# Kernel optimization log

Measured on AMD Instinct MI355X. Metric: run time of the kernel, lower is better.

## Reference

```python
import jax, jax.numpy as jnp
import numpy as np

N, M, D = 8192, 8192, 64

def softplus(x):
    # transform_forward in pmf-automl
    return jnp.logaddexp(x, 0.0)

def inv_softplus(y):
    # transform_backward: log(exp(y) - 1), stable form
    return y + jnp.log(-jnp.expm1(-y))

def setup_inputs() -> dict:
    key = jax.random.key(0)
    k1, k2 = jax.random.split(key)
    X = jax.random.normal(k1, (N, D), dtype=jnp.float32)
    X2 = jax.random.normal(k2, (M, D), dtype=jnp.float32)
    # raw (pre-softplus) parameters, matching torch init: softplus(raw)=1
    lengthscale = jnp.full((1, D), inv_softplus(jnp.float32(1.0)), dtype=jnp.float32)
    variance = jnp.full((1,), inv_softplus(jnp.float32(1.0)), dtype=jnp.float32)
    return {"X": X, "X2": X2, "lengthscale": lengthscale, "variance": variance}

def reference(X, X2, lengthscale, variance):
    l = softplus(lengthscale)           # [1, D]
    v = softplus(variance)              # [1]
    Xl = X / l                          # [N, D]
    X2l = X2 / l                        # [M, D]
    xn = jnp.sum(Xl * Xl, axis=1)       # [N]
    yn = jnp.sum(X2l * X2l, axis=1)     # [M]
    cross = Xl @ X2l.T                  # [N, M]
    d2 = jnp.maximum(xn[:, None] + yn[None, :] - 2.0 * cross, 0.0)
    return v[0] * jnp.exp(-0.5 * d2)
```

## Files before the change

### kernel.cpp

```cpp
#include <hip/hip_runtime.h>
#include <math.h>

#define NN 8192
#define MM 8192
#define DD 64
#define BM 128
#define BN 128
#define STR 72

typedef __bf16 bf16x8 __attribute__((ext_vector_type(8)));
typedef __bf16 bf16x4 __attribute__((ext_vector_type(4)));
typedef float f32x4 __attribute__((ext_vector_type(4)));

__device__ __forceinline__ float softplus_f(float x) {
    return fmaxf(x, 0.0f) + log1pf(exp2f(-fabsf(x) * 1.4426950408889634f));
}

__global__ __launch_bounds__(256, 2)
void rbf_mfma_kernel(const float* __restrict__ X, const float* __restrict__ X2,
                     const float* __restrict__ raw_l, const float* __restrict__ raw_v,
                     float* __restrict__ out) {
    __shared__ __bf16 Ah[BM][STR];
    __shared__ __bf16 Al[BM][STR];
    __shared__ __bf16 Bh[BN][STR];
    __shared__ __bf16 Bl[BN][STR];
    __shared__ float ls[DD];
    __shared__ float xn[BM];
    __shared__ float yn[BN];

    const int t  = threadIdx.x;
    const int bn = blockIdx.x;
    const int bm = blockIdx.y;

    if (t < DD) ls[t] = 1.0f / softplus_f(raw_l[t]);
    __syncthreads();

    const int k4 = t & 15;
    const int r0 = t >> 4;
    const float il0 = ls[4 * k4 + 0];
    const float il1 = ls[4 * k4 + 1];
    const float il2 = ls[4 * k4 + 2];
    const float il3 = ls[4 * k4 + 3];

    const float* Xb  = X  + (size_t)(bm * BM) * DD;
    const float* X2b = X2 + (size_t)(bn * BN) * DD;

#pragma unroll
    for (int r = 0; r < 8; ++r) {
        const int row = r0 + 16 * r;
        {
            float4 a = *(const float4*)(Xb + row * DD + 4 * k4);
            a.x *= il0; a.y *= il1; a.z *= il2; a.w *= il3;
            bf16x4 h, l;
            h[0] = (__bf16)a.x; l[0] = (__bf16)(a.x - (float)h[0]);
            h[1] = (__bf16)a.y; l[1] = (__bf16)(a.y - (float)h[1]);
            h[2] = (__bf16)a.z; l[2] = (__bf16)(a.z - (float)h[2]);
            h[3] = (__bf16)a.w; l[3] = (__bf16)(a.w - (float)h[3]);
            *(bf16x4*)&Ah[row][4 * k4] = h;
            *(bf16x4*)&Al[row][4 * k4] = l;
        }
        {
            float4 b = *(const float4*)(X2b + row * DD + 4 * k4);
            b.x *= il0; b.y *= il1; b.z *= il2; b.w *= il3;
            bf16x4 h, l;
            h[0] = (__bf16)b.x; l[0] = (__bf16)(b.x - (float)h[0]);
            h[1] = (__bf16)b.y; l[1] = (__bf16)(b.y - (float)h[1]);
            h[2] = (__bf16)b.z; l[2] = (__bf16)(b.z - (float)h[2]);
            h[3] = (__bf16)b.w; l[3] = (__bf16)(b.w - (float)h[3]);
            *(bf16x4*)&Bh[row][4 * k4] = h;
            *(bf16x4*)&Bl[row][4 * k4] = l;
        }
    }

    {
        const int rowl = t & 127;
        const float* p = (t < 128) ? (Xb + rowl * DD) : (X2b + rowl * DD);
        float s = 0.0f;
#pragma unroll
        for (int j = 0; j < 16; ++j) {
            float4 a = *(const float4*)(p + 4 * j);
            float e;
            e = a.x * ls[4 * j + 0]; s = fmaf(e, e, s);
            e = a.y * ls[4 * j + 1]; s = fmaf(e, e, s);
            e = a.z * ls[4 * j + 2]; s = fmaf(e, e, s);
            e = a.w * ls[4 * j + 3]; s = fmaf(e, e, s);
        }
        if (t < 128) xn[rowl] = s; else yn[rowl] = s;
    }
    __syncthreads();

    const int lane = t & 63;
    const int q    = lane >> 4;
    const int r16  = lane & 15;
    const int w    = t >> 6;
    const int row0 = (w >> 1) * 64;
    const int col0 = (w & 1) * 64;

    f32x4 acc[4][4];
#pragma unroll
    for (int mi = 0; mi < 4; ++mi)
#pragma unroll
        for (int ni = 0; ni < 4; ++ni)
#pragma unroll
            for (int r = 0; r < 4; ++r) acc[mi][ni][r] = 0.0f;

#pragma unroll
    for (int kc = 0; kc < 2; ++kc) {
        const int k0 = kc * 32 + q * 8;
        bf16x8 ah[4], al[4], bh[4], bl[4];
#pragma unroll
        for (int i = 0; i < 4; ++i) {
            ah[i] = *(const bf16x8*)&Ah[row0 + i * 16 + r16][k0];
            al[i] = *(const bf16x8*)&Al[row0 + i * 16 + r16][k0];
            bh[i] = *(const bf16x8*)&Bh[col0 + i * 16 + r16][k0];
            bl[i] = *(const bf16x8*)&Bl[col0 + i * 16 + r16][k0];
        }
#pragma unroll
        for (int mi = 0; mi < 4; ++mi) {
#pragma unroll
            for (int ni = 0; ni < 4; ++ni) {
                acc[mi][ni] = __builtin_amdgcn_mfma_f32_16x16x32_bf16(ah[mi], bh[ni], acc[mi][ni], 0, 0, 0);
                acc[mi][ni] = __builtin_amdgcn_mfma_f32_16x16x32_bf16(ah[mi], bl[ni], acc[mi][ni], 0, 0, 0);
                acc[mi][ni] = __builtin_amdgcn_mfma_f32_16x16x32_bf16(al[mi], bh[ni], acc[mi][ni], 0, 0, 0);
            }
        }
    }

    const float v  = softplus_f(raw_v[0]);
    const float ce = -0.5f * 1.4426950408889634f;

#pragma unroll
    for (int mi = 0; mi < 4; ++mi) {
#pragma unroll
        for (int r = 0; r < 4; ++r) {
            const int lrow = row0 + mi * 16 + q * 4 + r;
            const float xr = xn[lrow];
            float* orow = out + (size_t)(bm * BM + lrow) * MM + bn * BN;
#pragma unroll
            for (int ni = 0; ni < 4; ++ni) {
                const int lcol = col0 + ni * 16 + r16;
                float d2 = fmaxf(xr + yn[lcol] - 2.0f * acc[mi][ni][r], 0.0f);
                orow[lcol] = v * exp2f(ce * d2);
            }
        }
    }
}

extern "C" void kernel_launch(void* const* d_in, const int* in_sizes, int n_in,
                              void* d_out, int out_size, void* d_ws, size_t ws_size,
                              hipStream_t stream) {
    const float* X     = (const float*)d_in[0];
    const float* X2    = (const float*)d_in[1];
    const float* raw_l = (const float*)d_in[2];
    const float* raw_v = (const float*)d_in[3];
    float* out = (float*)d_out;

    dim3 grid(MM / BN, NN / BM);
    dim3 block(256);
    rbf_mfma_kernel<<<grid, block, 0, stream>>>(X, X2, raw_l, raw_v, out);
}
```

Measured before the change: 325.6 us.

## Precompute scaled bf16 hi/lo splits and norms in a prep kernel, stage output via LDS

A separate prep kernel scales X and X2 by the inverse lengthscale once, splits each into bf16 hi/lo parts, and computes the row norms into global scratch buffers. The GEMM kernel then reads its MFMA operands straight from global memory, with no per-tile conversion and no LDS operand staging. Operands are swapped in the MFMA so each lane holds contiguous output columns. Results go through a swizzled per-wave LDS tile so stores are coalesced 16-byte writes. This removes redundant per-block conversion work and the scattered 4-byte output stores, at the cost of an extra launch, global scratch traffic, and uncached-by-LDS operand loads.

```diff
diff --git a/kernel.cpp b/kernel.cpp
--- a/kernel.cpp
+++ b/kernel.cpp
@@ -6,95 +6,72 @@
 #define DD 64
 #define BM 128
 #define BN 128
-#define STR 72
 
 typedef __bf16 bf16x8 __attribute__((ext_vector_type(8)));
 typedef __bf16 bf16x4 __attribute__((ext_vector_type(4)));
 typedef float f32x4 __attribute__((ext_vector_type(4)));
 
+__device__ __align__(16) __bf16 g_Xh[(size_t)NN * DD];
+__device__ __align__(16) __bf16 g_Xl[(size_t)NN * DD];
+__device__ __align__(16) __bf16 g_Yh[(size_t)MM * DD];
+__device__ __align__(16) __bf16 g_Yl[(size_t)MM * DD];
+__device__ __align__(16) float  g_xn[NN];
+__device__ __align__(16) float  g_yn[MM];
+
 __device__ __forceinline__ float softplus_f(float x) {
     return fmaxf(x, 0.0f) + log1pf(exp2f(-fabsf(x) * 1.4426950408889634f));
 }
 
-__global__ __launch_bounds__(256, 2)
-void rbf_mfma_kernel(const float* __restrict__ X, const float* __restrict__ X2,
-                     const float* __restrict__ raw_l, const float* __restrict__ raw_v,
-                     float* __restrict__ out) {
-    __shared__ __bf16 Ah[BM][STR];
-    __shared__ __bf16 Al[BM][STR];
-    __shared__ __bf16 Bh[BN][STR];
-    __shared__ __bf16 Bl[BN][STR];
+__global__ __launch_bounds__(64)
+void prep_kernel(const float* __restrict__ X, const float* __restrict__ X2,
+                 const float* __restrict__ raw_l) {
     __shared__ float ls[DD];
-    __shared__ float xn[BM];
-    __shared__ float yn[BN];
-
-    const int t  = threadIdx.x;
-    const int bn = blockIdx.x;
-    const int bm = blockIdx.y;
-
-    if (t < DD) ls[t] = 1.0f / softplus_f(raw_l[t]);
+    const int t = threadIdx.x;
+    ls[t] = 1.0f / softplus_f(raw_l[t]);
     __syncthreads();
 
-    const int k4 = t & 15;
-    const int r0 = t >> 4;
-    const float il0 = ls[4 * k4 + 0];
-    const float il1 = ls[4 * k4 + 1];
-    const float il2 = ls[4 * k4 + 2];
-    const float il3 = ls[4 * k4 + 3];
+    const int row = blockIdx.x * 64 + t;
+    const bool isX = row < NN;
+    const int r = isX ? row : row - NN;
+    const float* src = (isX ? X : X2) + (size_t)r * DD;
+    __bf16* dh = (isX ? g_Xh : g_Yh) + (size_t)r * DD;
+    __bf16* dl = (isX ? g_Xl : g_Yl) + (size_t)r * DD;
 
-    const float* Xb  = X  + (size_t)(bm * BM) * DD;
-    const float* X2b = X2 + (size_t)(bn * BN) * DD;
+    float s = 0.0f;
+#pragma unroll
+    for (int j = 0; j < 16; ++j) {
+        float4 a = *(const float4*)(src + 4 * j);
+        a.x *= ls[4 * j + 0];
+        a.y *= ls[4 * j + 1];
+        a.z *= ls[4 * j + 2];
+        a.w *= ls[4 * j + 3];
+        bf16x4 h, l;
+        h[0] = (__bf16)a.x; l[0] = (__bf16)(a.x - (float)h[0]);
+        h[1] = (__bf16)a.y; l[1] = (__bf16)(a.y - (float)h[1]);
+        h[2] = (__bf16)a.z; l[2] = (__bf16)(a.z - (float)h[2]);
+        h[3] = (__bf16)a.w; l[3] = (__bf16)(a.w - (float)h[3]);
+        *(bf16x4*)(dh + 4 * j) = h;
+        *(bf16x4*)(dl + 4 * j) = l;
+        s = fmaf(a.x, a.x, s);
+        s = fmaf(a.y, a.y, s);
+        s = fmaf(a.z, a.z, s);
+        s = fmaf(a.w, a.w, s);
+    }
+    if (isX) g_xn[r] = s; else g_yn[r] = s;
+}
 
-#pragma unroll
-    for (int r = 0; r < 8; ++r) {
-        const int row = r0 + 16 * r;
-        {
-            float4 a = *(const float4*)(Xb + row * DD + 4 * k4);
-            a.x *= il0; a.y *= il1; a.z *= il2; a.w *= il3;
-            bf16x4 h, l;
-            h[0] = (__bf16)a.x; l[0] = (__bf16)(a.x - (float)h[0]);
-            h[1] = (__bf16)a.y; l[1] = (__bf16)(a.y - (float)h[1]);
-            h[2] = (__bf16)a.z; l[2] = (__bf16)(a.z - (float)h[2]);
-            h[3] = (__bf16)a.w; l[3] = (__bf16)(a.w - (float)h[3]);
-            *(bf16x4*)&Ah[row][4 * k4] = h;
-            *(bf16x4*)&Al[row][4 * k4] = l;
-        }
-        {
-            float4 b = *(const float4*)(X2b + row * DD + 4 * k4);
-            b.x *= il0; b.y *= il1; b.z *= il2; b.w *= il3;
-            bf16x4 h, l;
-            h[0] = (__bf16)b.x; l[0] = (__bf16)(b.x - (float)h[0]);
-            h[1] = (__bf16)b.y; l[1] = (__bf16)(b.y - (float)h[1]);
-            h[2] = (__bf16)b.z; l[2] = (__bf16)(b.z - (float)h[2]);
-            h[3] = (__bf16)b.w; l[3] = (__bf16)(b.w - (float)h[3]);
-            *(bf16x4*)&Bh[row][4 * k4] = h;
-            *(bf16x4*)&Bl[row][4 * k4] = l;
-        }
-    }
+__global__ __launch_bounds__(256, 2)
+void rbf_gemm_kernel(const float* __restrict__ raw_v, float* __restrict__ out) {
+    __shared__ __align__(16) float ctile[4][64 * 64];
 
-    {
-        const int rowl = t & 127;
-        const float* p = (t < 128) ? (Xb + rowl * DD) : (X2b + rowl * DD);
-        float s = 0.0f;
-#pragma unroll
-        for (int j = 0; j < 16; ++j) {
-            float4 a = *(const float4*)(p + 4 * j);
-            float e;
-            e = a.x * ls[4 * j + 0]; s = fmaf(e, e, s);
-            e = a.y * ls[4 * j + 1]; s = fmaf(e, e, s);
-            e = a.z * ls[4 * j + 2]; s = fmaf(e, e, s);
-            e = a.w * ls[4 * j + 3]; s = fmaf(e, e, s);
-        }
-        if (t < 128) xn[rowl] = s; else yn[rowl] = s;
-    }
-    __syncthreads();
-
+    const int t    = threadIdx.x;
     const int lane = t & 63;
+    const int w    = t >> 6;
     const int q    = lane >> 4;
     const int r16  = lane & 15;
-    const int w    = t >> 6;
-    const int row0 = (w >> 1) * 64;
-    const int col0 = (w & 1) * 64;
+
+    const int row0 = blockIdx.y * BM + (w >> 1) * 64;
+    const int col0 = blockIdx.x * BN + (w & 1) * 64;
 
     f32x4 acc[4][4];
 #pragma unroll
@@ -102,47 +79,70 @@
 #pragma unroll
         for (int ni = 0; ni < 4; ++ni)
 #pragma unroll
-            for (int r = 0; r < 4; ++r) acc[mi][ni][r] = 0.0f;
+            for (int rr = 0; rr < 4; ++rr) acc[mi][ni][rr] = 0.0f;
+
+    const char* Xh = (const char*)g_Xh;
+    const char* Xl = (const char*)g_Xl;
+    const char* Yh = (const char*)g_Yh;
+    const char* Yl = (const char*)g_Yl;
 
 #pragma unroll
     for (int kc = 0; kc < 2; ++kc) {
-        const int k0 = kc * 32 + q * 8;
+        const int kb = kc * 64 + q * 16;
         bf16x8 ah[4], al[4], bh[4], bl[4];
 #pragma unroll
         for (int i = 0; i < 4; ++i) {
-            ah[i] = *(const bf16x8*)&Ah[row0 + i * 16 + r16][k0];
-            al[i] = *(const bf16x8*)&Al[row0 + i * 16 + r16][k0];
-            bh[i] = *(const bf16x8*)&Bh[col0 + i * 16 + r16][k0];
-            bl[i] = *(const bf16x8*)&Bl[col0 + i * 16 + r16][k0];
+            const size_t ao = (size_t)(row0 + i * 16 + r16) * 128 + kb;
+            const size_t bo = (size_t)(col0 + i * 16 + r16) * 128 + kb;
+            ah[i] = *(const bf16x8*)(Xh + ao);
+            al[i] = *(const bf16x8*)(Xl + ao);
+            bh[i] = *(const bf16x8*)(Yh + bo);
+            bl[i] = *(const bf16x8*)(Yl + bo);
         }
 #pragma unroll
-        for (int mi = 0; mi < 4; ++mi) {
+        for (int mi = 0; mi < 4; ++mi)
 #pragma unroll
             for (int ni = 0; ni < 4; ++ni) {
-                acc[mi][ni] = __builtin_amdgcn_mfma_f32_16x16x32_bf16(ah[mi], bh[ni], acc[mi][ni], 0, 0, 0);
-                acc[mi][ni] = __builtin_amdgcn_mfma_f32_16x16x32_bf16(ah[mi], bl[ni], acc[mi][ni], 0, 0, 0);
-                acc[mi][ni] = __builtin_amdgcn_mfma_f32_16x16x32_bf16(al[mi], bh[ni], acc[mi][ni], 0, 0, 0);
+                acc[mi][ni] = __builtin_amdgcn_mfma_f32_16x16x32_bf16(bh[ni], ah[mi], acc[mi][ni], 0, 0, 0);
+                acc[mi][ni] = __builtin_amdgcn_mfma_f32_16x16x32_bf16(bl[ni], ah[mi], acc[mi][ni], 0, 0, 0);
+                acc[mi][ni] = __builtin_amdgcn_mfma_f32_16x16x32_bf16(bh[ni], al[mi], acc[mi][ni], 0, 0, 0);
             }
-        }
     }
 
     const float v  = softplus_f(raw_v[0]);
     const float ce = -0.5f * 1.4426950408889634f;
 
+    float xs[4];
+    f32x4 yn4[4];
+#pragma unroll
+    for (int mi = 0; mi < 4; ++mi) xs[mi] = g_xn[row0 + mi * 16 + r16];
+#pragma unroll
+    for (int ni = 0; ni < 4; ++ni) yn4[ni] = *(const f32x4*)(g_yn + col0 + ni * 16 + q * 4);
+
+    float* cw = ctile[w];
 #pragma unroll
     for (int mi = 0; mi < 4; ++mi) {
+        const int ml = mi * 16 + r16;
 #pragma unroll
-        for (int r = 0; r < 4; ++r) {
-            const int lrow = row0 + mi * 16 + q * 4 + r;
-            const float xr = xn[lrow];
-            float* orow = out + (size_t)(bm * BM + lrow) * MM + bn * BN;
+        for (int ni = 0; ni < 4; ++ni) {
+            f32x4 o;
 #pragma unroll
-            for (int ni = 0; ni < 4; ++ni) {
-                const int lcol = col0 + ni * 16 + r16;
-                float d2 = fmaxf(xr + yn[lcol] - 2.0f * acc[mi][ni][r], 0.0f);
-                orow[lcol] = v * exp2f(ce * d2);
+            for (int rr = 0; rr < 4; ++rr) {
+                float d2 = fmaxf(xs[mi] + yn4[ni][rr] - 2.0f * acc[mi][ni][rr], 0.0f);
+                o[rr] = v * exp2f(ce * d2);
             }
+            const int chs = (ni * 4 + q) ^ (ml & 7);
+            *(f32x4*)&cw[ml * 64 + chs * 4] = o;
         }
+    }
+
+#pragma unroll
+    for (int j = 0; j < 16; ++j) {
+        const int ml  = j * 4 + q;
+        const int chs = r16 ^ (ml & 7);
+        f32x4 o = *(const f32x4*)&cw[ml * 64 + chs * 4];
+        float* dst = out + (size_t)(row0 + ml) * MM + col0 + r16 * 4;
+        *(f32x4*)dst = o;
     }
 }
 
@@ -155,7 +155,6 @@
     const float* raw_v = (const float*)d_in[3];
     float* out = (float*)d_out;
 
-    dim3 grid(MM / BN, NN / BM);
-    dim3 block(256);
-    rbf_mfma_kernel<<<grid, block, 0, stream>>>(X, X2, raw_l, raw_v, out);
+    prep_kernel<<<dim3((NN + MM) / 64), dim3(64), 0, stream>>>(X, X2, raw_l);
+    rbf_gemm_kernel<<<dim3(MM / BN, NN / BM), dim3(256), 0, stream>>>(raw_v, out);
 }
```

New measurement: 302.1 us. 1.08x faster.
